# Kernel optimization log

Measured on AMD Instinct MI355X. Metric: run time of the kernel, lower is better.

Reference implementation:

```python
import math
import jax, jax.numpy as jnp
import numpy as np

B, S, D, H = 2, 2048, 1024, 16
HD = D // H  # 64


def setup_inputs() -> dict:
    key = jax.random.key(0)
    k = jax.random.split(key, 8)
    x = jax.random.normal(k[0], (B, S, D), dtype=jnp.float32)
    # RoPE tables: inv_freq over half dim, emb = concat(freqs, freqs)
    inv_freq = 1.0 / (10000.0 ** (jnp.arange(0, HD, 2, dtype=jnp.float32) / HD))
    pos = jnp.arange(S, dtype=jnp.float32)
    freqs = pos[:, None] * inv_freq[None, :]            # [S, HD/2]
    emb = jnp.concatenate([freqs, freqs], axis=-1)      # [S, HD]
    cos = jnp.cos(emb)[:, None, :]                      # [S, 1, HD] broadcasts over [B,S,H,HD]
    sin = jnp.sin(emb)[:, None, :]
    # causal additive mask [1, 1, S, S]
    neg = jnp.finfo(jnp.float32).min
    mask = jnp.where(jnp.tril(jnp.ones((S, S), dtype=bool)), 0.0, neg)[None, None]
    scale = 0.02
    wq = jax.random.normal(k[1], (D, D), dtype=jnp.float32) * scale
    wk = jax.random.normal(k[2], (D, D), dtype=jnp.float32) * scale
    wv = jax.random.normal(k[3], (D, D), dtype=jnp.float32) * scale
    wo = jax.random.normal(k[4], (D, D), dtype=jnp.float32) * scale
    return {"x": x, "cos": cos, "sin": sin, "mask": mask,
            "wq": wq, "wk": wk, "wv": wv, "wo": wo}


def rotate_half(t):
    t1, t2 = t[..., : t.shape[-1] // 2], t[..., t.shape[-1] // 2:]
    return jnp.concatenate([-t2, t1], axis=-1)


def reference(x, cos, sin, mask, wq, wk, wv, wo):
    b, s, d = x.shape
    # torch nn.Linear: y = x @ W^T  (W is [out, in])
    q = (x @ wq.T).reshape(b, s, H, HD)
    kk = (x @ wk.T).reshape(b, s, H, HD)
    v = (x @ wv.T).reshape(b, s, H, HD)
    q = q * cos + rotate_half(q) * sin
    kk = kk * cos + rotate_half(kk) * sin
    q = q.transpose(0, 2, 1, 3)   # [b, h, s, hd]
    kk = kk.transpose(0, 2, 1, 3)
    v = v.transpose(0, 2, 1, 3)
    scores = jnp.einsum('bhqd,bhkd->bhqk', q, kk) / math.sqrt(HD)
    scores = scores + mask
    probs = jax.nn.softmax(scores.astype(jnp.float32), axis=-1).astype(q.dtype)
    out = jnp.einsum('bhqk,bhkd->bhqd', probs, v)
    out = out.transpose(0, 2, 1, 3).reshape(b, s, d)
    return out @ wo.T
```

## Files before the change

### kernel.cpp

```cpp
#include <hip/hip_runtime.h>
#include <hip/hip_bf16.h>

typedef __hip_bfloat16 bf16;
typedef unsigned short u16;
typedef __attribute__((ext_vector_type(8))) short short8;
typedef __attribute__((ext_vector_type(4))) float floatx4;

constexpr int B_ = 2, S_ = 2048, D_ = 1024, H_ = 16, HD_ = 64;
constexpr int QT = 64, KT = 64, PAD = 72;
constexpr int NQT = S_ / QT;
constexpr int GK = 1024, BK = 64;

__device__ inline float b2f(u16 u) {
    union { unsigned int i; float f; } v; v.i = ((unsigned int)u) << 16; return v.f;
}
__device__ inline u16 f2b(float f) {
    bf16 h = __float2bfloat16(f); return *(u16*)&h;
}

__device__ inline void gl16(const u16* g, u16* l) {
    __builtin_amdgcn_global_load_lds(
        (const __attribute__((address_space(1))) unsigned int*)g,
        (__attribute__((address_space(3))) unsigned int*)l, 16, 0, 0);
}

__global__ __launch_bounds__(256) void cvt_kernel(
    const float* __restrict__ x,  const float* __restrict__ wq,
    const float* __restrict__ wk, const float* __restrict__ wv,
    const float* __restrict__ wo,
    u16* __restrict__ Xb, u16* __restrict__ Wb)
{
    const size_t c = (size_t)blockIdx.x * 256 + threadIdx.x;
    const float* src; u16* dst; size_t off;
    if (c < (size_t)(1 << 19)) { src = x; dst = Xb; off = c; }
    else {
        const size_t w = c - (1 << 19);
        const int wi = (int)(w >> 17);
        off = w & ((1 << 17) - 1);
        src = (wi == 0) ? wq : (wi == 1) ? wk : (wi == 2) ? wv : wo;
        dst = Wb + ((size_t)wi << 20);
    }
    const float4 a = *(const float4*)(src + off * 8);
    const float4 b = *(const float4*)(src + off * 8 + 4);
    ushort4 u0; u0.x = f2b(a.x); u0.y = f2b(a.y); u0.z = f2b(a.z); u0.w = f2b(a.w);
    ushort4 u1; u1.x = f2b(b.x); u1.y = f2b(b.y); u1.z = f2b(b.z); u1.w = f2b(b.w);
    *(ushort4*)(dst + off * 8)     = u0;
    *(ushort4*)(dst + off * 8 + 4) = u1;
}

template <typename TC, int SCATTER, int ROPE, int BN>
__global__ __launch_bounds__(256) void gemm_async(
    const u16* __restrict__ A, const u16* __restrict__ Wb,
    const float* __restrict__ cosp, const float* __restrict__ sinp,
    TC* __restrict__ C0, TC* __restrict__ C1, TC* __restrict__ C2, int N)
{
    constexpr int NT = BN / 32;

    int x, y, z;
    {
        const int xcd = blockIdx.x & 7, idx = blockIdx.x >> 3;
        y = (xcd & 3) * 8 + (idx & 7);
        if (BN == 128) {
            const int xz = (xcd >> 2) * 12 + (idx >> 3);
            x = xz & 7; z = xz >> 3;
        } else {
            x = (xcd >> 2) * 8 + (idx >> 3);
            z = 0;
        }
    }

    const u16* W = Wb + ((size_t)z << 20);
    TC*        C = (z == 0) ? C0 : (z == 1 ? C1 : C2);

    __shared__ __align__(16) u16 As[128 * BK];
    __shared__ __align__(16) u16 Bs[BN * BK];

    const int tid  = threadIdx.x;
    const int wave = tid >> 6, lane = tid & 63;
    const int quad = lane >> 4, l16 = lane & 15;
    const int wm = wave >> 1, wn = wave & 1;
    const int m0 = y * 128, n0 = x * BN;

    const int srl = lane >> 3;
    const int sc  = (lane & 7) ^ srl;

    floatx4 acc[4][NT] = {};

    for (int k0 = 0; k0 < GK; k0 += BK) {
        __syncthreads();
#pragma unroll
        for (int j = 0; j < 4; ++j) {
            const int rb = wave * 32 + j * 8;
            gl16(A + (size_t)(m0 + rb + srl) * GK + k0 + sc * 8, &As[rb * BK]);
        }
#pragma unroll
        for (int j = 0; j < BN / 32; ++j) {
            const int rb = wave * (BN / 4) + j * 8;
            gl16(W + (size_t)(n0 + rb + srl) * GK + k0 + sc * 8, &Bs[rb * BK]);
        }
        __syncthreads();

#pragma unroll
        for (int ks = 0; ks < 2; ++ks) {
            short8 af[4], bfr[NT];
#pragma unroll
            for (int mt = 0; mt < 4; ++mt) {
                const int R = wm * 64 + mt * 16 + l16;
                af[mt] = *(const short8*)&As[R * BK + (((ks * 4 + quad) ^ (l16 & 7)) * 8)];
            }
#pragma unroll
            for (int nt = 0; nt < NT; ++nt) {
                const int R = wn * (BN / 2) + nt * 16 + l16;
                bfr[nt] = *(const short8*)&Bs[R * BK + (((ks * 4 + quad) ^ (l16 & 7)) * 8)];
            }
#pragma unroll
            for (int mt = 0; mt < 4; ++mt)
#pragma unroll
                for (int nt = 0; nt < NT; ++nt)
                    acc[mt][nt] = __builtin_amdgcn_mfma_f32_16x16x32_bf16(
                        af[mt], bfr[nt], acc[mt][nt], 0, 0, 0);
        }
    }

    if (ROPE && z < 2) {
        float* Cs = (float*)As;
        float* Sn = (float*)Bs;
        const int s0 = m0 & (S_ - 1);
        const int bq = m0 >> 11;
        __syncthreads();
        {
            const int rr = tid >> 1;
            const int cc = (tid & 1) * 16;
            const float4* cp = (const float4*)(cosp + (size_t)(s0 + rr) * HD_ + cc);
            const float4* sp = (const float4*)(sinp + (size_t)(s0 + rr) * HD_ + cc);
            float4* cd = (float4*)&Cs[rr * 32 + cc];
            float4* sd = (float4*)&Sn[rr * 32 + cc];
            cd[0] = cp[0]; cd[1] = cp[1]; cd[2] = cp[2]; cd[3] = cp[3];
            sd[0] = sp[0]; sd[1] = sp[1]; sd[2] = sp[2]; sd[3] = sp[3];
        }
        __syncthreads();

        const float scale = (z == 0) ? 0.125f * 1.44269504f : 1.0f;
        const int h = (n0 >> 6) + wn;
#pragma unroll
        for (int mt = 0; mt < 4; ++mt)
#pragma unroll
            for (int r = 0; r < 4; ++r) {
                const int mr = wm * 64 + mt * 16 + quad * 4 + r;
                const size_t base = ((size_t)(bq * H_ + h) * S_ + s0 + mr) << 6;
#pragma unroll
                for (int np = 0; np < 2; ++np) {
                    const int d = np * 16 + l16;
                    const float c1 = Cs[mr * 32 + d];
                    const float s1 = Sn[mr * 32 + d];
                    const float q0 = acc[mt][np][r], q1 = acc[mt][np + 2][r];
                    ((bf16*)C)[base + d]      = __float2bfloat16((q0 * c1 - q1 * s1) * scale);
                    ((bf16*)C)[base + d + 32] = __float2bfloat16((q1 * c1 + q0 * s1) * scale);
                }
            }
    } else if (SCATTER) {
        const int s0 = m0 & (S_ - 1);
        const int bq = m0 >> 11;
        const int h  = (n0 >> 6) + wn;
        const int bh = bq * H_ + h;
#pragma unroll
        for (int mt = 0; mt < 4; ++mt)
#pragma unroll
            for (int nt = 0; nt < NT; ++nt) {
                const int hd = nt * 16 + l16;
                const int sb = s0 + wm * 64 + mt * 16 + quad * 4;
                ushort4 pk;
                pk.x = f2b(acc[mt][nt][0]); pk.y = f2b(acc[mt][nt][1]);
                pk.z = f2b(acc[mt][nt][2]); pk.w = f2b(acc[mt][nt][3]);
                *(ushort4*)&((u16*)C)[((size_t)(bh * HD_ + hd) << 11) + sb] = pk;
            }
    } else {
#pragma unroll
        for (int mt = 0; mt < 4; ++mt)
#pragma unroll
            for (int nt = 0; nt < NT; ++nt)
#pragma unroll
                for (int r = 0; r < 4; ++r) {
                    const int m = m0 + wm * 64 + mt * 16 + quad * 4 + r;
                    const int n = n0 + wn * (BN / 2) + nt * 16 + l16;
                    ((float*)C)[(size_t)m * N + n] = acc[mt][nt][r];
                }
    }
}

__global__ __launch_bounds__(256) void fa_kernel(
    const u16* __restrict__ Qg, const u16* __restrict__ Kg, const u16* __restrict__ Vt,
    bf16* __restrict__ Og)
{
    __shared__ __align__(16) u16 Kt[2][KT * PAD];
    __shared__ __align__(16) u16 Vs[2][HD_ * PAD];
    __shared__ __align__(16) u16 Pt[4 * 16 * PAD];

    const int flat = blockIdx.x;
    const int bx = flat >> 5;
    const int bh = flat & 31;
    const int b  = bh >> 4, h = bh & 15;
    const int tid  = threadIdx.x;
    const int wave = tid >> 6, lane = tid & 63;
    const int quad = lane >> 4, l16 = lane & 15;
    const int srow = tid >> 2, scol = (tid & 3) * 16;

    for (int half = 0; half < 2; ++half) {
        const int qt = half ? (NQT - 1 - bx) : bx;
        const int qb = qt * QT;

        const u16* qrow = Qg + ((size_t)bh * S_ + qb + wave * 16 + l16) * HD_;
        const short8 aq0 = *(const short8*)(qrow + quad * 8);
        const short8 aq1 = *(const short8*)(qrow + 32 + quad * 8);

        floatx4 oacc[4] = {{0,0,0,0},{0,0,0,0},{0,0,0,0},{0,0,0,0}};
        float lsum = 0.f;

        __syncthreads();
        {
            const u16* kp = Kg + ((size_t)bh * S_ + srow) * HD_ + scol;
            *(short8*)&Kt[0][srow * PAD + scol]     = *(const short8*)kp;
            *(short8*)&Kt[0][srow * PAD + scol + 8] = *(const short8*)(kp + 8);
            const u16* vp = Vt + ((size_t)bh * HD_ + srow) * S_ + scol;
            *(short8*)&Vs[0][srow * PAD + scol]     = *(const short8*)vp;
            *(short8*)&Vs[0][srow * PAD + scol + 8] = *(const short8*)(vp + 8);
        }
        __syncthreads();

        for (int it = 0; it <= qt; ++it) {
            const int  cur = it & 1;
            const bool pf  = (it < qt);
            short8 nk0, nk1, nv0, nv1;
            if (pf) {
                const int kb = (it + 1) * KT;
                const u16* kp = Kg + ((size_t)bh * S_ + kb + srow) * HD_ + scol;
                nk0 = *(const short8*)kp; nk1 = *(const short8*)(kp + 8);
                const u16* vp = Vt + ((size_t)bh * HD_ + srow) * S_ + kb + scol;
                nv0 = *(const short8*)vp; nv1 = *(const short8*)(vp + 8);
            }

            floatx4 sacc[4] = {{0,0,0,0},{0,0,0,0},{0,0,0,0},{0,0,0,0}};
#pragma unroll
            for (int kt = 0; kt < 4; ++kt) {
                const short8 bk0 = *(const short8*)&Kt[cur][(kt * 16 + l16) * PAD + quad * 8];
                const short8 bk1 = *(const short8*)&Kt[cur][(kt * 16 + l16) * PAD + 32 + quad * 8];
                sacc[kt] = __builtin_amdgcn_mfma_f32_16x16x32_bf16(bk0, aq0, sacc[kt], 0, 0, 0);
                sacc[kt] = __builtin_amdgcn_mfma_f32_16x16x32_bf16(bk1, aq1, sacc[kt], 0, 0, 0);
            }

            if (it == qt) {
                const int ql = wave * 16 + l16;
#pragma unroll
                for (int kt = 0; kt < 4; ++kt)
#pragma unroll
                    for (int r = 0; r < 4; ++r)
                        if (kt * 16 + quad * 4 + r > ql) sacc[kt][r] = -1.0e38f;
            }

            float rs = 0.f;
#pragma unroll
            for (int kt = 0; kt < 4; ++kt) {
                const float e0 = __builtin_amdgcn_exp2f(sacc[kt][0]);
                const float e1 = __builtin_amdgcn_exp2f(sacc[kt][1]);
                const float e2 = __builtin_amdgcn_exp2f(sacc[kt][2]);
                const float e3 = __builtin_amdgcn_exp2f(sacc[kt][3]);
                rs += (e0 + e1) + (e2 + e3);
                ushort4 pk; pk.x = f2b(e0); pk.y = f2b(e1); pk.z = f2b(e2); pk.w = f2b(e3);
                *(ushort4*)&Pt[(wave * 16 + l16) * PAD + kt * 16 + quad * 4] = pk;
            }
            rs += __shfl_xor(rs, 16);
            rs += __shfl_xor(rs, 32);
            lsum += rs;

            const short8 ap0 = *(const short8*)&Pt[(wave * 16 + l16) * PAD + quad * 8];
            const short8 ap1 = *(const short8*)&Pt[(wave * 16 + l16) * PAD + 32 + quad * 8];

#pragma unroll
            for (int dt = 0; dt < 4; ++dt) {
                const short8 bv0 = *(const short8*)&Vs[cur][(dt * 16 + l16) * PAD + quad * 8];
                const short8 bv1 = *(const short8*)&Vs[cur][(dt * 16 + l16) * PAD + 32 + quad * 8];
                oacc[dt] = __builtin_amdgcn_mfma_f32_16x16x32_bf16(bv0, ap0, oacc[dt], 0, 0, 0);
                oacc[dt] = __builtin_amdgcn_mfma_f32_16x16x32_bf16(bv1, ap1, oacc[dt], 0, 0, 0);
            }

            if (pf) {
                const int nb = cur ^ 1;
                *(short8*)&Kt[nb][srow * PAD + scol]     = nk0;
                *(short8*)&Kt[nb][srow * PAD + scol + 8] = nk1;
                *(short8*)&Vs[nb][srow * PAD + scol]     = nv0;
                *(short8*)&Vs[nb][srow * PAD + scol + 8] = nv1;
            }
            __syncthreads();
        }

        const float inv = 1.0f / lsum;
        bf16* orow = Og + ((size_t)(b * S_ + qb + wave * 16 + l16)) * D_ + h * HD_;
#pragma unroll
        for (int dt = 0; dt < 4; ++dt) {
            ushort4 pk;
            pk.x = f2b(oacc[dt][0] * inv);
            pk.y = f2b(oacc[dt][1] * inv);
            pk.z = f2b(oacc[dt][2] * inv);
            pk.w = f2b(oacc[dt][3] * inv);
            *(ushort4*)((u16*)orow + dt * 16 + quad * 4) = pk;
        }
    }
}

extern "C" void kernel_launch(void* const* d_in, const int* in_sizes, int n_in,
                              void* d_out, int out_size, void* d_ws, size_t ws_size,
                              hipStream_t stream)
{
    const float* x    = (const float*)d_in[0];
    const float* cosp = (const float*)d_in[1];
    const float* sinp = (const float*)d_in[2];
    const float* wq   = (const float*)d_in[4];
    const float* wk   = (const float*)d_in[5];
    const float* wv   = (const float*)d_in[6];
    const float* wo   = (const float*)d_in[7];
    float* out = (float*)d_out;

    u16* w0 = (u16*)d_ws;
    const size_t NE = (size_t)B_ * S_ * D_;
    u16* Qb  = w0;
    u16* Kb  = w0 + NE;
    u16* Vtb = w0 + 2 * NE;
    u16* Xb  = w0 + 3 * NE;
    u16* Wb  = w0 + 4 * NE;
    u16* Ab  = Xb;
    u16* Wob = Wb + 3 * (1 << 20);

    cvt_kernel<<<4096, 256, 0, stream>>>(x, wq, wk, wv, wo, Xb, Wb);

    gemm_async<bf16, 1, 1, 128><<<768, 256, 0, stream>>>(
        Xb, Wb, cosp, sinp, (bf16*)Qb, (bf16*)Kb, (bf16*)Vtb, D_);

    fa_kernel<<<dim3((NQT / 2) * 32, 1, 1), 256, 0, stream>>>(Qb, Kb, Vtb, (bf16*)Ab);

    gemm_async<float, 0, 0, 64><<<512, 256, 0, stream>>>(
        Ab, Wob, cosp, sinp, out, out, out, D_);
}
```

Measured before the change: 195.7 us.

## Replace QKV projection GEMM with 256x256-tile ping-pong scheduled kernel

Adds a dedicated QKV projection kernel that uses 256x256 output tiles, 8 waves per block and 128KB of dynamic LDS. Global-to-LDS async loads are staged in halves across a double buffer, with explicit barriers, waitcnts and setprio around MFMA phases to overlap loads with compute. RoPE and the V-transpose epilogues move into it, and the old generic gemm epilogue branches are emptied. The aim is more data reuse per tile and better load/compute overlap. The cost is only 192 blocks, which may leave many CUs idle on a 256-CU part.

Result: faster. 189.3 us (-3.3%).

```diff
diff --git a/kernel.cpp b/kernel.cpp
--- a/kernel.cpp
+++ b/kernel.cpp
@@ -23,6 +23,8 @@
         (const __attribute__((address_space(1))) unsigned int*)g,
         (__attribute__((address_space(3))) unsigned int*)l, 16, 0, 0);
 }
+
+#define SBAR() __builtin_amdgcn_sched_barrier(0)
 
 __global__ __launch_bounds__(256) void cvt_kernel(
     const float* __restrict__ x,  const float* __restrict__ wq,
@@ -48,6 +50,178 @@
     *(ushort4*)(dst + off * 8 + 4) = u1;
 }
 
+__global__ __launch_bounds__(512, 2) void qkv8(
+    const u16* __restrict__ Ag, const u16* __restrict__ Wall,
+    const float* __restrict__ cosp, const float* __restrict__ sinp,
+    bf16* __restrict__ Qo, bf16* __restrict__ Ko, u16* __restrict__ Vt)
+{
+    extern __shared__ u16 lds[];
+
+    const int wgid = (blockIdx.x & 7) * 24 + (blockIdx.x >> 3);
+    const int mt = wgid / 12;
+    const int rem = wgid - mt * 12;
+    const int nt = rem & 3, z = rem >> 2;
+
+    const u16* W = Wall + ((size_t)z << 20);
+    const int m0 = mt * 256, n0 = nt * 256;
+
+    const int tid  = threadIdx.x;
+    const int wave = tid >> 6, lane = tid & 63;
+    const int quad = lane >> 4, l16 = lane & 15;
+    const int wm = wave >> 2, wn = wave & 3;
+
+    const int lr_st = wave * 16 + (lane >> 2);
+    const int csrc  = ((lane & 3) ^ ((lane >> 5) << 1)) * 8;
+    const int grA   = ((lr_st >> 6) << 7) + (lr_st & 63);
+    const int grB   = ((lr_st >> 5) << 6) + (lr_st & 31);
+
+    const int cidx = ((quad ^ (((l16 >> 3) & 1) << 1))) * 8;
+
+    floatx4 acc[8][4] = {};
+    short8 af[4][2], bA[2][2], bB[2][2];
+
+    const u16* A_st = Ag + (size_t)(m0 + grA) * GK + csrc;
+    const u16* B_st = W  + (size_t)(n0 + grB) * GK + csrc;
+
+    auto stA = [&](int t2, int mh) {
+        if (t2 > 15) return;
+        const u16* s = A_st + ((size_t)mh * 64) * GK + t2 * 64;
+        u16* d = lds + (((t2 & 1) * 2 + mh) * 8192) + wave * 512;
+        gl16(s, d);
+        gl16(s + 32, d + 4096);
+    };
+    auto stB = [&](int t2, int nh) {
+        if (t2 > 15) return;
+        const u16* s = B_st + ((size_t)nh * 32) * GK + t2 * 64;
+        u16* d = lds + 32768 + (((t2 & 1) * 2 + nh) * 8192) + wave * 512;
+        gl16(s, d);
+        gl16(s + 32, d + 4096);
+    };
+    auto rdA = [&](int sl, int mh) {
+        const int base = (sl * 2 + mh) * 8192 + cidx;
+#pragma unroll
+        for (int mf = 0; mf < 4; ++mf) {
+            const int lr = wm * 64 + mf * 16 + l16;
+#pragma unroll
+            for (int ks = 0; ks < 2; ++ks)
+                af[mf][ks] = *(const short8*)&lds[base + ks * 4096 + lr * 32];
+        }
+    };
+    auto rdB = [&](short8 (&bf)[2][2], int sl, int nh) {
+        const int base = 32768 + (sl * 2 + nh) * 8192 + cidx;
+#pragma unroll
+        for (int fn = 0; fn < 2; ++fn) {
+            const int lr = wn * 32 + fn * 16 + l16;
+#pragma unroll
+            for (int ks = 0; ks < 2; ++ks)
+                bf[fn][ks] = *(const short8*)&lds[base + ks * 4096 + lr * 32];
+        }
+    };
+    auto mm = [&](int mh, int nh, short8 (&bf)[2][2]) {
+#pragma unroll
+        for (int mf = 0; mf < 4; ++mf)
+#pragma unroll
+            for (int fn = 0; fn < 2; ++fn)
+#pragma unroll
+                for (int ks = 0; ks < 2; ++ks)
+                    acc[mh * 4 + mf][nh * 2 + fn] =
+                        __builtin_amdgcn_mfma_f32_16x16x32_bf16(
+                            af[mf][ks], bf[fn][ks],
+                            acc[mh * 4 + mf][nh * 2 + fn], 0, 0, 0);
+    };
+
+    stA(0, 0); stB(0, 0); stA(0, 1); stB(0, 1); stA(1, 0); stB(1, 0);
+    asm volatile("s_waitcnt vmcnt(4)" ::: "memory");
+    SBAR(); __builtin_amdgcn_s_barrier(); SBAR();
+
+    for (int t = 0; t < 16; ++t) {
+        const int sl = t & 1;
+        rdA(sl, 0); rdB(bA, sl, 0); stA(t + 1, 1);
+        SBAR(); __builtin_amdgcn_s_barrier();
+        asm volatile("s_waitcnt lgkmcnt(0)" ::: "memory"); SBAR();
+        __builtin_amdgcn_s_setprio(1);
+        mm(0, 0, bA);
+        __builtin_amdgcn_s_setprio(0);
+        SBAR(); __builtin_amdgcn_s_barrier(); SBAR();
+        rdB(bB, sl, 1); stB(t + 1, 1);
+        SBAR(); __builtin_amdgcn_s_barrier();
+        asm volatile("s_waitcnt lgkmcnt(0)" ::: "memory"); SBAR();
+        __builtin_amdgcn_s_setprio(1);
+        mm(0, 1, bB);
+        __builtin_amdgcn_s_setprio(0);
+        SBAR(); __builtin_amdgcn_s_barrier(); SBAR();
+        rdA(sl, 1); stA(t + 2, 0);
+        SBAR(); __builtin_amdgcn_s_barrier();
+        asm volatile("s_waitcnt lgkmcnt(0)" ::: "memory"); SBAR();
+        __builtin_amdgcn_s_setprio(1);
+        mm(1, 0, bA);
+        __builtin_amdgcn_s_setprio(0);
+        SBAR(); __builtin_amdgcn_s_barrier(); SBAR();
+        stB(t + 2, 0);
+        SBAR(); __builtin_amdgcn_s_barrier();
+        asm volatile("s_waitcnt lgkmcnt(0)" ::: "memory"); SBAR();
+        __builtin_amdgcn_s_setprio(1);
+        mm(1, 1, bB);
+        __builtin_amdgcn_s_setprio(0);
+        SBAR();
+        if (t < 14)       asm volatile("s_waitcnt vmcnt(4)" ::: "memory");
+        else if (t == 14) asm volatile("s_waitcnt vmcnt(0)" ::: "memory");
+        SBAR(); __builtin_amdgcn_s_barrier(); SBAR();
+    }
+
+    const int s0 = m0 & (S_ - 1);
+    const int bq = m0 >> 11;
+    const int h  = (n0 >> 6) + wn;
+
+    if (z < 2) {
+        float* Cs = (float*)lds;
+        float* Sn = (float*)(lds + 16384);
+        {
+            const int rr = tid >> 1;
+            const int cc = (tid & 1) * 16;
+            const float4* cp = (const float4*)(cosp + (size_t)(s0 + rr) * HD_ + cc);
+            const float4* sp = (const float4*)(sinp + (size_t)(s0 + rr) * HD_ + cc);
+            float4* cd = (float4*)&Cs[rr * 32 + cc];
+            float4* sd = (float4*)&Sn[rr * 32 + cc];
+            cd[0] = cp[0]; cd[1] = cp[1]; cd[2] = cp[2]; cd[3] = cp[3];
+            sd[0] = sp[0]; sd[1] = sp[1]; sd[2] = sp[2]; sd[3] = sp[3];
+        }
+        __syncthreads();
+
+        const float scale = (z == 0) ? 0.125f * 1.44269504f : 1.0f;
+        bf16* C = (z == 0) ? Qo : Ko;
+#pragma unroll
+        for (int mf = 0; mf < 8; ++mf)
+#pragma unroll
+            for (int r = 0; r < 4; ++r) {
+                const int mr = wm * 128 + mf * 16 + quad * 4 + r;
+                const size_t base = ((size_t)(bq * H_ + h) * S_ + s0 + mr) << 6;
+#pragma unroll
+                for (int np = 0; np < 2; ++np) {
+                    const int d = np * 16 + l16;
+                    const float c1 = Cs[mr * 32 + d];
+                    const float s1 = Sn[mr * 32 + d];
+                    const float q0 = acc[mf][np][r], q1 = acc[mf][np + 2][r];
+                    C[base + d]      = __float2bfloat16((q0 * c1 - q1 * s1) * scale);
+                    C[base + d + 32] = __float2bfloat16((q1 * c1 + q0 * s1) * scale);
+                }
+            }
+    } else {
+        const int bh = bq * H_ + h;
+#pragma unroll
+        for (int mf = 0; mf < 8; ++mf)
+#pragma unroll
+            for (int nf = 0; nf < 4; ++nf) {
+                const int hd = nf * 16 + l16;
+                const int sb = s0 + wm * 128 + mf * 16 + quad * 4;
+                ushort4 pk;
+                pk.x = f2b(acc[mf][nf][0]); pk.y = f2b(acc[mf][nf][1]);
+                pk.z = f2b(acc[mf][nf][2]); pk.w = f2b(acc[mf][nf][3]);
+                *(ushort4*)&Vt[((size_t)(bh * HD_ + hd) << 11) + sb] = pk;
+            }
+    }
+}
+
 template <typename TC, int SCATTER, int ROPE, int BN>
 __global__ __launch_bounds__(256) void gemm_async(
     const u16* __restrict__ A, const u16* __restrict__ Wb,
@@ -123,57 +297,7 @@
     }
 
     if (ROPE && z < 2) {
-        float* Cs = (float*)As;
-        float* Sn = (float*)Bs;
-        const int s0 = m0 & (S_ - 1);
-        const int bq = m0 >> 11;
-        __syncthreads();
-        {
-            const int rr = tid >> 1;
-            const int cc = (tid & 1) * 16;
-            const float4* cp = (const float4*)(cosp + (size_t)(s0 + rr) * HD_ + cc);
-            const float4* sp = (const float4*)(sinp + (size_t)(s0 + rr) * HD_ + cc);
-            float4* cd = (float4*)&Cs[rr * 32 + cc];
-            float4* sd = (float4*)&Sn[rr * 32 + cc];
-            cd[0] = cp[0]; cd[1] = cp[1]; cd[2] = cp[2]; cd[3] = cp[3];
-            sd[0] = sp[0]; sd[1] = sp[1]; sd[2] = sp[2]; sd[3] = sp[3];
-        }
-        __syncthreads();
-
-        const float scale = (z == 0) ? 0.125f * 1.44269504f : 1.0f;
-        const int h = (n0 >> 6) + wn;
-#pragma unroll
-        for (int mt = 0; mt < 4; ++mt)
-#pragma unroll
-            for (int r = 0; r < 4; ++r) {
-                const int mr = wm * 64 + mt * 16 + quad * 4 + r;
-                const size_t base = ((size_t)(bq * H_ + h) * S_ + s0 + mr) << 6;
-#pragma unroll
-                for (int np = 0; np < 2; ++np) {
-                    const int d = np * 16 + l16;
-                    const float c1 = Cs[mr * 32 + d];
-                    const float s1 = Sn[mr * 32 + d];
-                    const float q0 = acc[mt][np][r], q1 = acc[mt][np + 2][r];
-                    ((bf16*)C)[base + d]      = __float2bfloat16((q0 * c1 - q1 * s1) * scale);
-                    ((bf16*)C)[base + d + 32] = __float2bfloat16((q1 * c1 + q0 * s1) * scale);
-                }
-            }
     } else if (SCATTER) {
-        const int s0 = m0 & (S_ - 1);
-        const int bq = m0 >> 11;
-        const int h  = (n0 >> 6) + wn;
-        const int bh = bq * H_ + h;
-#pragma unroll
-        for (int mt = 0; mt < 4; ++mt)
-#pragma unroll
-            for (int nt = 0; nt < NT; ++nt) {
-                const int hd = nt * 16 + l16;
-                const int sb = s0 + wm * 64 + mt * 16 + quad * 4;
-                ushort4 pk;
-                pk.x = f2b(acc[mt][nt][0]); pk.y = f2b(acc[mt][nt][1]);
-                pk.z = f2b(acc[mt][nt][2]); pk.w = f2b(acc[mt][nt][3]);
-                *(ushort4*)&((u16*)C)[((size_t)(bh * HD_ + hd) << 11) + sb] = pk;
-            }
     } else {
 #pragma unroll
         for (int mt = 0; mt < 4; ++mt)
@@ -330,10 +454,17 @@
     u16* Ab  = Xb;
     u16* Wob = Wb + 3 * (1 << 20);
 
+    static bool inited = false;
+    if (!inited) {
+        hipFuncSetAttribute((const void*)qkv8,
+                            hipFuncAttributeMaxDynamicSharedMemorySize, 131072);
+        inited = true;
+    }
+
     cvt_kernel<<<4096, 256, 0, stream>>>(x, wq, wk, wv, wo, Xb, Wb);
 
-    gemm_async<bf16, 1, 1, 128><<<768, 256, 0, stream>>>(
-        Xb, Wb, cosp, sinp, (bf16*)Qb, (bf16*)Kb, (bf16*)Vtb, D_);
+    qkv8<<<192, 512, 131072, stream>>>(
+        Xb, Wb, cosp, sinp, (bf16*)Qb, (bf16*)Kb, Vtb);
 
     fa_kernel<<<dim3((NQT / 2) * 32, 1, 1), 256, 0, stream>>>(Qb, Kb, Vtb, (bf16*)Ab);
 
```
